# Kernel tuning notes

Measured on AMD Instinct MI355X. Metric: run time of the kernel, lower is better.

Reference implementation:

```python
import jax, jax.numpy as jnp
import numpy as np

N = 50000      # nodes
E = 400000     # edges (before self loops)
F_IN = 128     # num_features
HID = 64       # hidden_dim
HEADS = 4
G = 64         # number of graphs in batch
NCLS = 2
NEG = 0.2      # leaky relu negative slope
BN_EPS = 1e-5


def setup_inputs() -> dict:
    key = jax.random.key(0)
    ks = jax.random.split(key, 32)
    rn = lambda k, shape, s=0.05: jax.random.normal(k, shape, jnp.float32) * s
    inp = {}
    inp["x"] = jax.random.normal(ks[0], (N, F_IN), jnp.float32)
    inp["edge_index"] = jax.random.randint(ks[1], (2, E), 0, N, dtype=jnp.int32)
    inp["batch"] = jnp.sort(jax.random.randint(ks[2], (N,), 0, G, dtype=jnp.int32))
    # layer 0 GATConv (concat=True) + pre projection
    inp["conv0_W"] = rn(ks[3], (F_IN, HEADS * HID))
    inp["conv0_att_src"] = rn(ks[4], (HEADS, HID))
    inp["conv0_att_dst"] = rn(ks[5], (HEADS, HID))
    inp["conv0_bias"] = jnp.zeros((HEADS * HID,), jnp.float32)
    inp["pre0_W"] = rn(ks[6], (HEADS * HID, HID))
    inp["pre0_b"] = jnp.zeros((HID,), jnp.float32)
    # layers 1..2 GATConv (concat=False), stacked
    inp["convs_W"] = rn(ks[7], (2, HID, HEADS * HID))
    inp["convs_att_src"] = rn(ks[8], (2, HEADS, HID))
    inp["convs_att_dst"] = rn(ks[9], (2, HEADS, HID))
    inp["convs_bias"] = jnp.zeros((2, HID), jnp.float32)
    # batch norms (eval mode: running stats)
    inp["bn_gamma"] = jnp.ones((3, HID), jnp.float32)
    inp["bn_beta"] = jnp.zeros((3, HID), jnp.float32)
    inp["bn_mean"] = rn(ks[10], (3, HID), 0.1)
    inp["bn_var"] = jax.random.uniform(ks[11], (3, HID), jnp.float32) + 0.5
    # JK projection, attention pooling, classifier
    inp["jump_W"] = rn(ks[12], (3 * HID, HID))
    inp["jump_b"] = jnp.zeros((HID,), jnp.float32)
    inp["att_W"] = rn(ks[13], (HID, 1))
    inp["att_b"] = jnp.zeros((1,), jnp.float32)
    inp["cls_W1"] = rn(ks[14], (HID, HID // 2))
    inp["cls_b1"] = jnp.zeros((HID // 2,), jnp.float32)
    inp["cls_W2"] = rn(ks[15], (HID // 2, NCLS))
    inp["cls_b2"] = jnp.zeros((NCLS,), jnp.float32)
    return inp


def _segment_softmax(logits, seg, num_segments):
    m = jax.ops.segment_max(logits, seg, num_segments=num_segments)
    e = jnp.exp(logits - m[seg])
    s = jax.ops.segment_sum(e, seg, num_segments=num_segments)
    return e / s[seg]


def _gat_conv(x, src, dst, W, a_src, a_dst, bias, concat):
    n = x.shape[0]
    H, C = a_src.shape
    xh = (x @ W).reshape(n, H, C)                         # [N, H, C]
    as_n = jnp.einsum('nhc,hc->nh', xh, a_src)            # [N, H]
    ad_n = jnp.einsum('nhc,hc->nh', xh, a_dst)            # [N, H]
    logits = jax.nn.leaky_relu(as_n[src] + ad_n[dst], NEG)  # [E', H]
    att = _segment_softmax(logits, dst, n)                # softmax over incoming edges
    out = jax.ops.segment_sum(xh[src] * att[:, :, None], dst, num_segments=n)
    out = out.reshape(n, H * C) if concat else out.mean(axis=1)
    return out + bias


def _bn(h, g, b, m, v):
    return (h - m) * jax.lax.rsqrt(v + BN_EPS) * g + b


def reference(x, edge_index, batch, conv0_W, conv0_att_src, conv0_att_dst,
              conv0_bias, pre0_W, pre0_b, convs_W, convs_att_src, convs_att_dst,
              convs_bias, bn_gamma, bn_beta, bn_mean, bn_var, jump_W, jump_b,
              att_W, att_b, cls_W1, cls_b1, cls_W2, cls_b2):
    n = x.shape[0]
    loops = jnp.arange(n, dtype=edge_index.dtype)
    src = jnp.concatenate([edge_index[0], loops])         # add_self_loops=True
    dst = jnp.concatenate([edge_index[1], loops])
    reps = []
    # layer 0: concat heads -> pre projection -> BN -> ELU (no residual: 128 != 64)
    h = _gat_conv(x, src, dst, conv0_W, conv0_att_src, conv0_att_dst, conv0_bias, True)
    h = h @ pre0_W + pre0_b
    h = jax.nn.elu(_bn(h, bn_gamma[0], bn_beta[0], bn_mean[0], bn_var[0]))
    reps.append(h)
    # layers 1..2: mean heads -> BN -> ELU -> residual
    for i in range(2):
        h_in = h
        h = _gat_conv(h, src, dst, convs_W[i], convs_att_src[i], convs_att_dst[i],
                      convs_bias[i], False)
        h = jax.nn.elu(_bn(h, bn_gamma[i + 1], bn_beta[i + 1], bn_mean[i + 1], bn_var[i + 1]))
        h = h + h_in
        reps.append(h)
    # jumping knowledge (cat)
    h = jnp.concatenate(reps, axis=-1) @ jump_W + jump_b  # [N, HID]
    # attentional global pooling
    a = _segment_softmax((h @ att_W + att_b)[:, 0], batch, G)  # [N]
    hg = jax.ops.segment_sum(h * a[:, None], batch, num_segments=G)  # [G, HID]
    # classifier
    return jax.nn.relu(hg @ cls_W1 + cls_b1) @ cls_W2 + cls_b2
```

## Files before the change

### kernel.cpp

```cpp
#include <hip/hip_runtime.h>
#include <hip/hip_bf16.h>
#include <math.h>

#define NEG 0.2f
#define BNEPS 1e-5f
#define NGRAPH 64
#define SCAN_CHUNK 2048
#define POOL_BLOCKS 256

typedef short bf16x8 __attribute__((ext_vector_type(8)));
typedef float f32x4  __attribute__((ext_vector_type(4)));
typedef float f32x2  __attribute__((ext_vector_type(2)));

__device__ __forceinline__ float bf2f(unsigned short u) {
    return __uint_as_float(((unsigned)u) << 16);
}
__device__ __forceinline__ short f2bf(float f) {
    return (short)__bfloat16_as_ushort(__float2bfloat16(f));
}
__device__ __forceinline__ unsigned char f2fp8(float f) {
    int pk = __builtin_amdgcn_cvt_pk_fp8_f32(f, f, 0, false);
    return (unsigned char)(pk & 0xFF);
}

__global__ __launch_bounds__(256)
void init_kernel(const int* __restrict__ batch, int N,
                 int* __restrict__ counts, int* __restrict__ gstart,
                 float* __restrict__ hg_acc, float* __restrict__ wsum_acc,
                 const float* __restrict__ convs_W,
                 const float* __restrict__ convs_as, const float* __restrict__ convs_ad,
                 float* __restrict__ uv)
{
    int idx = blockIdx.x * 256 + threadIdx.x;
    for (int i = idx; i < N; i += gridDim.x * 256) counts[i] = 0;
    if (blockIdx.x == 0) {
        int t = threadIdx.x;
        for (int i = t; i < NGRAPH * 64; i += 256) hg_acc[i] = 0.f;
        if (t < NGRAPH) wsum_acc[t] = 0.f;
        if (t <= NGRAPH) {
            int lo = 0, hi = N;
            while (lo < hi) {
                int mid = (lo + hi) >> 1;
                if (batch[mid] < t) lo = mid + 1; else hi = mid;
            }
            gstart[t] = lo;
        }
    }
    if (blockIdx.x == 1) {
        int t = threadIdx.x;
        int h = t >> 6, k = t & 63;
        for (int i = 0; i < 2; ++i) {
            const float* Wr  = convs_W + (size_t)i * 64 * 256 + k * 256 + h * 64;
            const float* av  = convs_as + i * 256 + h * 64;
            const float* dv  = convs_ad + i * 256 + h * 64;
            float su = 0.f, sv = 0.f;
            for (int c = 0; c < 64; ++c) { su += Wr[c] * av[c]; sv += Wr[c] * dv[c]; }
            uv[i * 256 + h * 64 + k]       = su;
            uv[512 + i * 256 + h * 64 + k] = sv;
        }
    }
}

__global__ __launch_bounds__(256)
void gemm_xh_mfma(const float* __restrict__ A, int lda,
                  const float* __restrict__ W, int Nc, int M, int K,
                  const float* __restrict__ att_s, const float* __restrict__ att_d,
                  float* __restrict__ as_out, float* __restrict__ ad_out,
                  unsigned char* __restrict__ C8)
{
    __shared__ short Wt[64 * 136];
    const int KP = K + 8;
    int tid  = threadIdx.x;
    int lane = tid & 63, wave = tid >> 6;
    int row0 = blockIdx.x * 64;
    int colb = blockIdx.y * 64;
    int c15 = lane & 15, q = lane >> 4;

    {
        int n = tid & 63;
        for (int k = tid >> 6; k < K; k += 4)
            Wt[n * KP + k] = f2bf(W[(size_t)k * Nc + colb + n]);
    }
    __syncthreads();

    int row = row0 + wave * 16 + c15;
    bool rok = row < M;
    const float* arow = A + (size_t)row * lda + q * 8;

    f32x4 acc[4];
    #pragma unroll
    for (int st = 0; st < 4; ++st) acc[st] = (f32x4){0.f, 0.f, 0.f, 0.f};

    for (int k0 = 0; k0 < K; k0 += 32) {
        bf16x8 av;
        if (rok) {
            float4 a0 = *(const float4*)(arow + k0);
            float4 a1 = *(const float4*)(arow + k0 + 4);
            av[0] = f2bf(a0.x); av[1] = f2bf(a0.y); av[2] = f2bf(a0.z); av[3] = f2bf(a0.w);
            av[4] = f2bf(a1.x); av[5] = f2bf(a1.y); av[6] = f2bf(a1.z); av[7] = f2bf(a1.w);
        } else {
            av = (bf16x8){0,0,0,0,0,0,0,0};
        }
        #pragma unroll
        for (int st = 0; st < 4; ++st) {
            bf16x8 bv = *(const bf16x8*)(Wt + (st * 16 + c15) * KP + k0 + q * 8);
            acc[st] = __builtin_amdgcn_mfma_f32_16x16x32_bf16(av, bv, acc[st], 0, 0, 0);
        }
    }

    #pragma unroll
    for (int r = 0; r < 4; ++r) {
        int orow = row0 + wave * 16 + q * 4 + r;
        if (orow >= M) continue;
        unsigned char* cb = C8 + (size_t)orow * 256 + colb + c15;
        #pragma unroll
        for (int st = 0; st < 4; ++st)
            cb[st * 16] = f2fp8(acc[st][r]);
    }
    float sa[4], da[4];
    #pragma unroll
    for (int st = 0; st < 4; ++st) {
        sa[st] = att_s[colb + st * 16 + c15];
        da[st] = att_d[colb + st * 16 + c15];
    }
    #pragma unroll
    for (int r = 0; r < 4; ++r) {
        float ps = acc[0][r] * sa[0] + acc[1][r] * sa[1] + acc[2][r] * sa[2] + acc[3][r] * sa[3];
        float pd = acc[0][r] * da[0] + acc[1][r] * da[1] + acc[2][r] * da[2] + acc[3][r] * da[3];
        #pragma unroll
        for (int o = 1; o < 16; o <<= 1) {
            ps += __shfl_xor(ps, o);
            pd += __shfl_xor(pd, o);
        }
        int orow = row0 + wave * 16 + q * 4 + r;
        if (c15 == 0 && orow < M) {
            as_out[orow * 4 + blockIdx.y] = ps;
            ad_out[orow * 4 + blockIdx.y] = pd;
        }
    }
}

__global__ __launch_bounds__(256)
void gemm_n64_mfma(const void* __restrict__ Araw, int lda, int a_is_bf16,
                   const float* __restrict__ W, int w_gat, int M, int K,
                   const float* __restrict__ bias, float scale,
                   float* __restrict__ C, int ldc, int mode,
                   const float* __restrict__ bn_g, const float* __restrict__ bn_b,
                   const float* __restrict__ bn_m, const float* __restrict__ bn_v,
                   const float* __restrict__ resid, int ldr,
                   unsigned char* __restrict__ h8_out,
                   const float* __restrict__ u, const float* __restrict__ v,
                   float* __restrict__ as_out, float* __restrict__ ad_out,
                   const float* __restrict__ attW, const float* __restrict__ attb,
                   float* __restrict__ wout)
{
    __shared__ short Wt[64 * 264];
    const int KP = K + 8;
    int tid  = threadIdx.x;
    int lane = tid & 63, wave = tid >> 6;
    int row0 = blockIdx.x * 64;
    int c15 = lane & 15, q = lane >> 4;

    {
        int n = tid & 63;
        for (int k = tid >> 6; k < K; k += 4) {
            int widx = w_gat ? ((k & 63) * 256 + (k >> 6) * 64 + n) : (k * 64 + n);
            Wt[n * KP + k] = f2bf(W[widx]);
        }
    }
    __syncthreads();

    int row = row0 + wave * 16 + c15;
    bool rok = row < M;

    f32x4 acc[4];
    #pragma unroll
    for (int st = 0; st < 4; ++st) acc[st] = (f32x4){0.f, 0.f, 0.f, 0.f};

    for (int k0 = 0; k0 < K; k0 += 32) {
        bf16x8 av;
        if (rok) {
            if (a_is_bf16) {
                av = *(const bf16x8*)((const unsigned short*)Araw
                                      + (size_t)row * lda + k0 + q * 8);
            } else {
                const float* ap = (const float*)Araw + (size_t)row * lda + k0 + q * 8;
                float4 a0 = *(const float4*)ap;
                float4 a1 = *(const float4*)(ap + 4);
                av[0] = f2bf(a0.x); av[1] = f2bf(a0.y); av[2] = f2bf(a0.z); av[3] = f2bf(a0.w);
                av[4] = f2bf(a1.x); av[5] = f2bf(a1.y); av[6] = f2bf(a1.z); av[7] = f2bf(a1.w);
            }
        } else {
            av = (bf16x8){0,0,0,0,0,0,0,0};
        }
        #pragma unroll
        for (int st = 0; st < 4; ++st) {
            bf16x8 bv = *(const bf16x8*)(Wt + (st * 16 + c15) * KP + k0 + q * 8);
            acc[st] = __builtin_amdgcn_mfma_f32_16x16x32_bf16(av, bv, acc[st], 0, 0, 0);
        }
    }

    #pragma unroll
    for (int st = 0; st < 4; ++st) {
        int col = st * 16 + c15;
        float bs = bias ? bias[col] : 0.f;
        float sg = 1.f, sb = 0.f;
        if (mode == 1) {
            sg = bn_g[col] / sqrtf(bn_v[col] + BNEPS);
            sb = bn_b[col] - bn_m[col] * sg;
        }
        #pragma unroll
        for (int r = 0; r < 4; ++r) {
            int orow = row0 + wave * 16 + q * 4 + r;
            if (orow >= M) continue;
            float vvv = acc[st][r] * scale + bs;
            if (mode == 1) {
                vvv = vvv * sg + sb;
                vvv = vvv > 0.f ? vvv : __expf(vvv) - 1.f;
            }
            if (resid) vvv += resid[(size_t)orow * ldr + col];
            acc[st][r] = vvv;
            C[(size_t)orow * ldc + col] = vvv;
        }
    }

    if (h8_out) {
        #pragma unroll
        for (int r = 0; r < 4; ++r) {
            int orow = row0 + wave * 16 + q * 4 + r;
            if (orow >= M) continue;
            unsigned char* hb = h8_out + (size_t)orow * 64 + c15;
            #pragma unroll
            for (int st = 0; st < 4; ++st)
                hb[st * 16] = f2fp8(acc[st][r]);
        }
    }

    if (u) {
        float uu[4][4], vv2[4][4];
        #pragma unroll
        for (int h = 0; h < 4; ++h)
            #pragma unroll
            for (int st = 0; st < 4; ++st) {
                uu[h][st]  = u[h * 64 + st * 16 + c15];
                vv2[h][st] = v[h * 64 + st * 16 + c15];
            }
        #pragma unroll
        for (int r = 0; r < 4; ++r) {
            int orow = row0 + wave * 16 + q * 4 + r;
            float pv[8];
            #pragma unroll
            for (int h = 0; h < 4; ++h) {
                pv[h]     = acc[0][r] * uu[h][0] + acc[1][r] * uu[h][1]
                          + acc[2][r] * uu[h][2] + acc[3][r] * uu[h][3];
                pv[4 + h] = acc[0][r] * vv2[h][0] + acc[1][r] * vv2[h][1]
                          + acc[2][r] * vv2[h][2] + acc[3][r] * vv2[h][3];
            }
            #pragma unroll
            for (int jj = 0; jj < 8; ++jj)
                #pragma unroll
                for (int o = 1; o < 16; o <<= 1) pv[jj] += __shfl_xor(pv[jj], o);
            if (c15 == 0 && orow < M) {
                #pragma unroll
                for (int h = 0; h < 4; ++h) {
                    as_out[orow * 4 + h] = pv[h];
                    ad_out[orow * 4 + h] = pv[4 + h];
                }
            }
        }
    }

    if (wout) {
        float sa[4];
        #pragma unroll
        for (int st = 0; st < 4; ++st) sa[st] = attW[st * 16 + c15];
        float ab = attb[0];
        #pragma unroll
        for (int r = 0; r < 4; ++r) {
            float ps = acc[0][r] * sa[0] + acc[1][r] * sa[1]
                     + acc[2][r] * sa[2] + acc[3][r] * sa[3];
            #pragma unroll
            for (int o = 1; o < 16; o <<= 1) ps += __shfl_xor(ps, o);
            int orow = row0 + wave * 16 + q * 4 + r;
            if (c15 == 0 && orow < M) wout[orow] = __expf(ps + ab);
        }
    }
}

__global__ __launch_bounds__(256)
void hist_kernel(const int* __restrict__ ei, int E, int N, int* __restrict__ counts)
{
    int e = blockIdx.x * blockDim.x + threadIdx.x;
    int Etot = E + N;
    if (e >= Etot) return;
    int d = (e < E) ? ei[E + e] : e - E;
    atomicAdd(&counts[d], 1);
}

__global__ __launch_bounds__(256)
void scan_phase1(const int* __restrict__ counts, int N, int* __restrict__ blocksum)
{
    __shared__ int wsum[4];
    int tid = threadIdx.x, lane = tid & 63, wave = tid >> 6;
    int base = blockIdx.x * SCAN_CHUNK;
    int s = 0;
    #pragma unroll
    for (int j = 0; j < SCAN_CHUNK / 256; ++j) {
        int idx = base + tid + j * 256;
        if (idx < N) s += counts[idx];
    }
    #pragma unroll
    for (int o = 32; o; o >>= 1) s += __shfl_xor(s, o);
    if (lane == 0) wsum[wave] = s;
    __syncthreads();
    if (tid == 0) blocksum[blockIdx.x] = wsum[0] + wsum[1] + wsum[2] + wsum[3];
}

__global__ __launch_bounds__(256)
void scan_phase3(const int* __restrict__ counts, int N, int nb,
                 const int* __restrict__ blocksum,
                 int* __restrict__ rowptr, int* __restrict__ cursor)
{
    __shared__ int wsum[4];
    __shared__ int pref[64];
    int tid = threadIdx.x, lane = tid & 63, wave = tid >> 6;

    if (wave == 0) {
        int v = (lane < nb) ? blocksum[lane] : 0;
        int incl = v;
        #pragma unroll
        for (int o = 1; o < 64; o <<= 1) {
            int t = __shfl_up(incl, o);
            if (lane >= o) incl += t;
        }
        pref[lane] = incl;
    }
    __syncthreads();
    int boff = blockIdx.x ? pref[blockIdx.x - 1] : 0;
    if (blockIdx.x == 0 && tid == 0) rowptr[N] = pref[nb - 1];

    int start = blockIdx.x * SCAN_CHUNK + tid * 8;
    int v[8];
    int s = 0;
    #pragma unroll
    for (int j = 0; j < 8; ++j) {
        v[j] = (start + j < N) ? counts[start + j] : 0;
        s += v[j];
    }
    int incl = s;
    #pragma unroll
    for (int o = 1; o < 64; o <<= 1) {
        int t = __shfl_up(incl, o);
        if (lane >= o) incl += t;
    }
    if (lane == 63) wsum[wave] = incl;
    __syncthreads();
    int woff = 0;
    #pragma unroll
    for (int w = 0; w < 4; ++w) if (w < wave) woff += wsum[w];
    int run = boff + woff + incl - s;
    #pragma unroll
    for (int j = 0; j < 8; ++j) {
        int idx = start + j;
        if (idx < N) { rowptr[idx] = run; cursor[idx] = run; }
        run += v[j];
    }
}

__global__ __launch_bounds__(256)
void scatter_kernel(const int* __restrict__ ei, int E, int N,
                    int* __restrict__ cursor, int* __restrict__ csr_src)
{
    int e = blockIdx.x * blockDim.x + threadIdx.x;
    int Etot = E + N;
    if (e >= Etot) return;
    int s, d;
    if (e < E) { s = ei[e]; d = ei[E + e]; } else { s = d = e - E; }
    int pos = atomicAdd(&cursor[d], 1);
    csr_src[pos] = s;
}

__global__ __launch_bounds__(256)
void aggregate_kernel(const int* __restrict__ rowptr, const int* __restrict__ csr_src,
                      const float* __restrict__ as_n, const float* __restrict__ ad_n,
                      const unsigned char* __restrict__ xh8,
                      const float* __restrict__ bias,
                      unsigned short* __restrict__ outp, int N)
{
    int node = (blockIdx.x * blockDim.x + threadIdx.x) >> 6;
    int lane = threadIdx.x & 63;
    if (node >= N) return;
    int h = lane >> 4, li = lane & 15, grp = lane & 48;
    int e0 = rowptr[node], e1 = rowptr[node + 1];
    float adh = ad_n[node * 4 + h];
    unsigned laneoff = (unsigned)(lane * 4);

    float4 acc = make_float4(0.f, 0.f, 0.f, 0.f);
    float wsum = 0.f;

    for (int base = e0; base < e1; base += 16) {
        int cnt = e1 - base; if (cnt > 16) cnt = 16;
        int s = 0; float w = 0.f;
        if (li < cnt) {
            s = csr_src[base + li];
            float l = as_n[s * 4 + h] + adh;
            l = fmaxf(l, NEG * l);
            w = __expf(l);
        }
        int k = 0;
        for (; k + 3 < cnt; k += 4) {
            float w0 = __shfl(w, grp + k),     w1 = __shfl(w, grp + k + 1);
            float w2 = __shfl(w, grp + k + 2), w3 = __shfl(w, grp + k + 3);
            int s0 = __shfl(s, grp + k),       s1 = __shfl(s, grp + k + 1);
            int s2 = __shfl(s, grp + k + 2),   s3 = __shfl(s, grp + k + 3);
            unsigned x0 = *(const unsigned*)(xh8 + ((unsigned)s0 * 256u + laneoff));
            unsigned x1 = *(const unsigned*)(xh8 + ((unsigned)s1 * 256u + laneoff));
            unsigned x2 = *(const unsigned*)(xh8 + ((unsigned)s2 * 256u + laneoff));
            unsigned x3 = *(const unsigned*)(xh8 + ((unsigned)s3 * 256u + laneoff));
            f32x2 l0 = __builtin_amdgcn_cvt_pk_f32_fp8((int)x0, false);
            f32x2 h0 = __builtin_amdgcn_cvt_pk_f32_fp8((int)x0, true);
            f32x2 l1 = __builtin_amdgcn_cvt_pk_f32_fp8((int)x1, false);
            f32x2 h1 = __builtin_amdgcn_cvt_pk_f32_fp8((int)x1, true);
            f32x2 l2 = __builtin_amdgcn_cvt_pk_f32_fp8((int)x2, false);
            f32x2 h2 = __builtin_amdgcn_cvt_pk_f32_fp8((int)x2, true);
            f32x2 l3 = __builtin_amdgcn_cvt_pk_f32_fp8((int)x3, false);
            f32x2 h3 = __builtin_amdgcn_cvt_pk_f32_fp8((int)x3, true);
            acc.x += w0 * l0.x; acc.y += w0 * l0.y; acc.z += w0 * h0.x; acc.w += w0 * h0.y;
            acc.x += w1 * l1.x; acc.y += w1 * l1.y; acc.z += w1 * h1.x; acc.w += w1 * h1.y;
            acc.x += w2 * l2.x; acc.y += w2 * l2.y; acc.z += w2 * h2.x; acc.w += w2 * h2.y;
            acc.x += w3 * l3.x; acc.y += w3 * l3.y; acc.z += w3 * h3.x; acc.w += w3 * h3.y;
            wsum += (w0 + w1) + (w2 + w3);
        }
        for (; k < cnt; ++k) {
            float wk = __shfl(w, grp + k);
            int sk = __shfl(s, grp + k);
            unsigned xv = *(const unsigned*)(xh8 + ((unsigned)sk * 256u + laneoff));
            f32x2 lo = __builtin_amdgcn_cvt_pk_f32_fp8((int)xv, false);
            f32x2 hi = __builtin_amdgcn_cvt_pk_f32_fp8((int)xv, true);
            acc.x += wk * lo.x; acc.y += wk * lo.y;
            acc.z += wk * hi.x; acc.w += wk * hi.y;
            wsum += wk;
        }
    }

    float rw = 1.f / wsum;
    float4 bs = *(const float4*)(bias + lane * 4);
    ushort4 pk;
    pk.x = (unsigned short)f2bf(acc.x * rw + bs.x);
    pk.y = (unsigned short)f2bf(acc.y * rw + bs.y);
    pk.z = (unsigned short)f2bf(acc.z * rw + bs.z);
    pk.w = (unsigned short)f2bf(acc.w * rw + bs.w);
    *(ushort4*)(outp + (size_t)node * 256 + lane * 4) = pk;
}

__global__ __launch_bounds__(256)
void aggregate_z(const int* __restrict__ rowptr, const int* __restrict__ csr_src,
                 const float* __restrict__ as_n, const float* __restrict__ ad_n,
                 const unsigned char* __restrict__ h8,
                 unsigned short* __restrict__ zout, int N)
{
    int node = (blockIdx.x * blockDim.x + threadIdx.x) >> 6;
    int lane = threadIdx.x & 63;
    if (node >= N) return;
    int g = lane >> 4, li = lane & 15, grp = lane & 48;
    int e0 = rowptr[node], e1 = rowptr[node + 1];
    float adh = ad_n[node * 4 + g];

    float acc[4][4];
    #pragma unroll
    for (int h = 0; h < 4; ++h)
        #pragma unroll
        for (int j = 0; j < 4; ++j) acc[h][j] = 0.f;
    float wsum = 0.f;

    for (int base = e0; base < e1; base += 16) {
        int cnt = e1 - base; if (cnt > 16) cnt = 16;
        int s = 0; float w = 0.f;
        if (li < cnt) {
            s = csr_src[base + li];
            float l = as_n[s * 4 + g] + adh;
            l = fmaxf(l, NEG * l);
            w = __expf(l);
        }
        wsum += w;
        for (int k = 0; k < cnt; k += 4) {
            int m = k + g;
            int   sm = __shfl(s, grp + m);
            float w0 = __shfl(w, m);
            float w1 = __shfl(w, 16 + m);
            float w2 = __shfl(w, 32 + m);
            float w3 = __shfl(w, 48 + m);
            if (m < cnt) {
                unsigned xv = *(const unsigned*)(h8 + ((unsigned)sm * 64u + (unsigned)(li * 4)));
                f32x2 lo = __builtin_amdgcn_cvt_pk_f32_fp8((int)xv, false);
                f32x2 hi = __builtin_amdgcn_cvt_pk_f32_fp8((int)xv, true);
                float f0 = lo.x, f1 = lo.y, f2 = hi.x, f3 = hi.y;
                acc[0][0] += w0 * f0; acc[0][1] += w0 * f1; acc[0][2] += w0 * f2; acc[0][3] += w0 * f3;
                acc[1][0] += w1 * f0; acc[1][1] += w1 * f1; acc[1][2] += w1 * f2; acc[1][3] += w1 * f3;
                acc[2][0] += w2 * f0; acc[2][1] += w2 * f1; acc[2][2] += w2 * f2; acc[2][3] += w2 * f3;
                acc[3][0] += w3 * f0; acc[3][1] += w3 * f1; acc[3][2] += w3 * f2; acc[3][3] += w3 * f3;
            }
        }
    }

    #pragma unroll
    for (int o = 1; o < 16; o <<= 1) wsum += __shfl_xor(wsum, o);
    #pragma unroll
    for (int h = 0; h < 4; ++h)
        #pragma unroll
        for (int j = 0; j < 4; ++j) {
            acc[h][j] += __shfl_xor(acc[h][j], 16);
            acc[h][j] += __shfl_xor(acc[h][j], 32);
        }
    float rw = 1.f / wsum;
    ushort4 pk;
    pk.x = (unsigned short)f2bf(acc[g][0] * rw);
    pk.y = (unsigned short)f2bf(acc[g][1] * rw);
    pk.z = (unsigned short)f2bf(acc[g][2] * rw);
    pk.w = (unsigned short)f2bf(acc[g][3] * rw);
    *(ushort4*)(zout + (size_t)node * 256 + g * 64 + li * 4) = pk;
}

__global__ __launch_bounds__(256)
void pool_partial(const float* __restrict__ hjk, const float* __restrict__ w,
                  const int* __restrict__ batch, const int* __restrict__ gstart,
                  float* __restrict__ hg_acc, float* __restrict__ wsum_acc, int N)
{
    __shared__ float red[256];
    __shared__ float wred[4];
    int tid = threadIdx.x;
    int c = tid & 63, q = tid >> 6;
    int slab = (N + POOL_BLOCKS - 1) / POOL_BLOCKS;
    int n0 = blockIdx.x * slab;
    int n1 = n0 + slab; if (n1 > N) n1 = N;
    if (n0 >= n1) return;
    int g0 = batch[n0], g1 = batch[n1 - 1];

    for (int g = g0; g <= g1; ++g) {
        int s = gstart[g];     if (s < n0) s = n0;
        int e = gstart[g + 1]; if (e > n1) e = n1;
        float acc = 0.f, ws = 0.f;
        for (int n = s + q; n < e; n += 4) {
            float wn = w[n];
            acc += wn * hjk[(size_t)n * 64 + c];
            if (c == 0) ws += wn;
        }
        red[tid] = acc;
        if (c == 0) wred[q] = ws;
        __syncthreads();
        if (q == 0) {
            float v = red[c] + red[64 + c] + red[128 + c] + red[192 + c];
            if (v != 0.f) atomicAdd(&hg_acc[g * 64 + c], v);
            if (c == 0) {
                float t = wred[0] + wred[1] + wred[2] + wred[3];
                if (t != 0.f) atomicAdd(&wsum_acc[g], t);
            }
        }
        __syncthreads();
    }
}

__global__ void cls_kernel(const float* __restrict__ hg_acc,
                           const float* __restrict__ wsum_acc,
                           const float* __restrict__ W1, const float* __restrict__ b1,
                           const float* __restrict__ W2, const float* __restrict__ b2,
                           float* __restrict__ out)
{
    int g = blockIdx.x, t = threadIdx.x;
    __shared__ float z[32];
    __shared__ float h[64];
    float wsum = wsum_acc[g];
    float rw = (wsum > 0.f) ? 1.f / wsum : 0.f;
    h[t] = hg_acc[g * 64 + t] * rw;
    h[t + 32] = hg_acc[g * 64 + t + 32] * rw;
    __syncthreads();
    float acc = b1[t];
    for (int k = 0; k < 64; ++k) acc += h[k] * W1[k * 32 + t];
    z[t] = fmaxf(acc, 0.f);
    __syncthreads();
    if (t < 2) {
        float o = b2[t];
        for (int j = 0; j < 32; ++j) o += z[j] * W2[j * 2 + t];
        out[g * 2 + t] = o;
    }
}

extern "C" void kernel_launch(void* const* d_in, const int* in_sizes, int n_in,
                              void* d_out, int out_size, void* d_ws, size_t ws_size,
                              hipStream_t stream)
{
    const float* x        = (const float*)d_in[0];
    const int*   ei       = (const int*)d_in[1];
    const int*   batch    = (const int*)d_in[2];
    const float* conv0_W  = (const float*)d_in[3];
    const float* conv0_as = (const float*)d_in[4];
    const float* conv0_ad = (const float*)d_in[5];
    const float* conv0_b  = (const float*)d_in[6];
    const float* pre0_W   = (const float*)d_in[7];
    const float* pre0_b   = (const float*)d_in[8];
    const float* convs_W  = (const float*)d_in[9];
    const float* convs_as = (const float*)d_in[10];
    const float* convs_ad = (const float*)d_in[11];
    const float* convs_b  = (const float*)d_in[12];
    const float* bn_g     = (const float*)d_in[13];
    const float* bn_b     = (const float*)d_in[14];
    const float* bn_m     = (const float*)d_in[15];
    const float* bn_v     = (const float*)d_in[16];
    const float* jump_W   = (const float*)d_in[17];
    const float* jump_b   = (const float*)d_in[18];
    const float* att_W    = (const float*)d_in[19];
    const float* att_b    = (const float*)d_in[20];
    const float* cls_W1   = (const float*)d_in[21];
    const float* cls_b1   = (const float*)d_in[22];
    const float* cls_W2   = (const float*)d_in[23];
    const float* cls_b2   = (const float*)d_in[24];
    float* out = (float*)d_out;

    const int N = in_sizes[0] / 128;
    const int E = in_sizes[1] / 2;
    const int Etot = E + N;
    const int nb = (N + SCAN_CHUNK - 1) / SCAN_CHUNK;

    float* ws      = (float*)d_ws;
    unsigned char* xh8      = (unsigned char*)ws;
    unsigned short* h256_bf = (unsigned short*)ws + (size_t)N * 256;
    float* repsAll = (float*)(h256_bf + (size_t)N * 256);
    float* as_n    = repsAll + (size_t)N * 192;
    float* ad_n    = as_n + (size_t)N * 4;
    float* hjk     = ad_n + (size_t)N * 4;
    float* hg_acc  = hjk + (size_t)N * 64;
    float* wsum_acc= hg_acc + NGRAPH * 64;
    int*   rowptr  = (int*)(wsum_acc + NGRAPH);
    int*   cursor  = rowptr + (N + 1);
    int*   counts  = cursor + N;
    int*   csr_src = counts + N;
    int*   gstart  = csr_src + Etot;
    int*   blocksum = gstart + (NGRAPH + 1);
    float* uv      = (float*)(blocksum + 64);
    unsigned char* h8 = xh8;
    float* wbuf    = as_n;

    dim3 blk(256);
    int node_wave_blocks = (N + 3) / 4;
    int edge_blocks      = (Etot + 255) / 256;
    int row_blocks       = (N + 63) / 64;

    init_kernel<<<64, blk, 0, stream>>>(batch, N, counts, gstart, hg_acc, wsum_acc,
                                        convs_W, convs_as, convs_ad, uv);
    hist_kernel<<<edge_blocks, blk, 0, stream>>>(ei, E, N, counts);
    scan_phase1<<<nb, blk, 0, stream>>>(counts, N, blocksum);
    scan_phase3<<<nb, blk, 0, stream>>>(counts, N, nb, blocksum, rowptr, cursor);
    scatter_kernel<<<edge_blocks, blk, 0, stream>>>(ei, E, N, cursor, csr_src);

    {
        dim3 g1(row_blocks, 4);
        gemm_xh_mfma<<<g1, blk, 0, stream>>>(x, 128, conv0_W, 256, N, 128,
                                             conv0_as, conv0_ad, as_n, ad_n, xh8);
        aggregate_kernel<<<node_wave_blocks, blk, 0, stream>>>(
            rowptr, csr_src, as_n, ad_n, xh8, conv0_b, h256_bf, N);
        gemm_n64_mfma<<<row_blocks, blk, 0, stream>>>(
            h256_bf, 256, 1, pre0_W, 0, N, 256, pre0_b, 1.f,
            repsAll, 192, 1, bn_g, bn_b, bn_m, bn_v,
            nullptr, 0, h8, uv, uv + 512, as_n, ad_n,
            nullptr, nullptr, nullptr);
    }

    aggregate_z<<<node_wave_blocks, blk, 0, stream>>>(rowptr, csr_src, as_n, ad_n,
                                                      h8, h256_bf, N);
    gemm_n64_mfma<<<row_blocks, blk, 0, stream>>>(
        h256_bf, 256, 1, convs_W, 1, N, 256, convs_b, 0.25f,
        repsAll + 64, 192, 1, bn_g + 64, bn_b + 64, bn_m + 64, bn_v + 64,
        repsAll, 192, h8, uv + 256, uv + 512 + 256, as_n, ad_n,
        nullptr, nullptr, nullptr);

    aggregate_z<<<node_wave_blocks, blk, 0, stream>>>(rowptr, csr_src, as_n, ad_n,
                                                      h8, h256_bf, N);
    gemm_n64_mfma<<<row_blocks, blk, 0, stream>>>(
        h256_bf, 256, 1, convs_W + (size_t)64 * 256, 1, N, 256, convs_b + 64, 0.25f,
        repsAll + 128, 192, 1, bn_g + 128, bn_b + 128, bn_m + 128, bn_v + 128,
        repsAll + 64, 192, nullptr, nullptr, nullptr, nullptr, nullptr,
        nullptr, nullptr, nullptr);

    gemm_n64_mfma<<<row_blocks, blk, 0, stream>>>(
        repsAll, 192, 0, jump_W, 0, N, 192, jump_b, 1.f,
        hjk, 64, 0, nullptr, nullptr, nullptr, nullptr,
        nullptr, 0, nullptr, nullptr, nullptr, nullptr, nullptr,
        att_W, att_b, wbuf);

    pool_partial<<<POOL_BLOCKS, blk, 0, stream>>>(hjk, wbuf, batch, gstart,
                                                  hg_acc, wsum_acc, N);
    cls_kernel<<<NGRAPH, 32, 0, stream>>>(hg_acc, wsum_acc, cls_W1, cls_b1,
                                          cls_W2, cls_b2, out);
}
```

Measured before the change: 394.5 us.

## Restructure aggregate_z to per-head lane groups and reduce attention dot shuffles

The aggregation kernel now gives each 16-lane group one head. Every group walks all edges with the same source rows, unrolled by four, so no cross-group accumulator reduction is needed and the register footprint drops from 16 accumulators to 4. In exchange each group issues four times as many gathers per edge and runs a serial per-edge loop. Separately, the GEMM epilogue replaces eight full 16-lane butterfly reductions with a recursive-halving transpose-reduce that leaves each lane holding one of the eight attention sums. This cuts the shuffle count in that epilogue.

```diff
diff --git a/kernel.cpp b/kernel.cpp
--- a/kernel.cpp
+++ b/kernel.cpp
@@ -257,15 +257,27 @@
                           + acc[2][r] * vv2[h][2] + acc[3][r] * vv2[h][3];
             }
             #pragma unroll
-            for (int jj = 0; jj < 8; ++jj)
-                #pragma unroll
-                for (int o = 1; o < 16; o <<= 1) pv[jj] += __shfl_xor(pv[jj], o);
-            if (c15 == 0 && orow < M) {
-                #pragma unroll
-                for (int h = 0; h < 4; ++h) {
-                    as_out[orow * 4 + h] = pv[h];
-                    ad_out[orow * 4 + h] = pv[4 + h];
-                }
+            for (int j = 0; j < 4; ++j) {
+                float send = (c15 & 8) ? pv[j] : pv[j + 4];
+                float keep = (c15 & 8) ? pv[j + 4] : pv[j];
+                pv[j] = keep + __shfl_xor(send, 8);
+            }
+            #pragma unroll
+            for (int j = 0; j < 2; ++j) {
+                float send = (c15 & 4) ? pv[j] : pv[j + 2];
+                float keep = (c15 & 4) ? pv[j + 2] : pv[j];
+                pv[j] = keep + __shfl_xor(send, 4);
+            }
+            {
+                float send = (c15 & 2) ? pv[0] : pv[1];
+                float keep = (c15 & 2) ? pv[1] : pv[0];
+                pv[0] = keep + __shfl_xor(send, 2);
+            }
+            pv[0] += __shfl_xor(pv[0], 1);
+            if ((c15 & 1) == 0 && orow < M) {
+                int jj = c15 >> 1;
+                if (jj < 4) as_out[orow * 4 + jj] = pv[0];
+                else        ad_out[orow * 4 + (jj - 4)] = pv[0];
             }
         }
     }
@@ -462,15 +474,12 @@
     int node = (blockIdx.x * blockDim.x + threadIdx.x) >> 6;
     int lane = threadIdx.x & 63;
     if (node >= N) return;
-    int g = lane >> 4, li = lane & 15, grp = lane & 48;
+    int h = lane >> 4, li = lane & 15, grp = lane & 48;
     int e0 = rowptr[node], e1 = rowptr[node + 1];
-    float adh = ad_n[node * 4 + g];
-
-    float acc[4][4];
-    #pragma unroll
-    for (int h = 0; h < 4; ++h)
-        #pragma unroll
-        for (int j = 0; j < 4; ++j) acc[h][j] = 0.f;
+    float adh = ad_n[node * 4 + h];
+    unsigned laneoff = (unsigned)(li * 4);
+
+    float4 acc = make_float4(0.f, 0.f, 0.f, 0.f);
     float wsum = 0.f;
 
     for (int base = e0; base < e1; base += 16) {
@@ -478,47 +487,53 @@
         int s = 0; float w = 0.f;
         if (li < cnt) {
             s = csr_src[base + li];
-            float l = as_n[s * 4 + g] + adh;
+            float l = as_n[s * 4 + h] + adh;
             l = fmaxf(l, NEG * l);
             w = __expf(l);
         }
-        wsum += w;
-        for (int k = 0; k < cnt; k += 4) {
-            int m = k + g;
-            int   sm = __shfl(s, grp + m);
-            float w0 = __shfl(w, m);
-            float w1 = __shfl(w, 16 + m);
-            float w2 = __shfl(w, 32 + m);
-            float w3 = __shfl(w, 48 + m);
-            if (m < cnt) {
-                unsigned xv = *(const unsigned*)(h8 + ((unsigned)sm * 64u + (unsigned)(li * 4)));
-                f32x2 lo = __builtin_amdgcn_cvt_pk_f32_fp8((int)xv, false);
-                f32x2 hi = __builtin_amdgcn_cvt_pk_f32_fp8((int)xv, true);
-                float f0 = lo.x, f1 = lo.y, f2 = hi.x, f3 = hi.y;
-                acc[0][0] += w0 * f0; acc[0][1] += w0 * f1; acc[0][2] += w0 * f2; acc[0][3] += w0 * f3;
-                acc[1][0] += w1 * f0; acc[1][1] += w1 * f1; acc[1][2] += w1 * f2; acc[1][3] += w1 * f3;
-                acc[2][0] += w2 * f0; acc[2][1] += w2 * f1; acc[2][2] += w2 * f2; acc[2][3] += w2 * f3;
-                acc[3][0] += w3 * f0; acc[3][1] += w3 * f1; acc[3][2] += w3 * f2; acc[3][3] += w3 * f3;
-            }
-        }
-    }
-
-    #pragma unroll
-    for (int o = 1; o < 16; o <<= 1) wsum += __shfl_xor(wsum, o);
-    #pragma unroll
-    for (int h = 0; h < 4; ++h)
-        #pragma unroll
-        for (int j = 0; j < 4; ++j) {
-            acc[h][j] += __shfl_xor(acc[h][j], 16);
-            acc[h][j] += __shfl_xor(acc[h][j], 32);
-        }
+        int k = 0;
+        for (; k + 3 < cnt; k += 4) {
+            float w0 = __shfl(w, grp + k),     w1 = __shfl(w, grp + k + 1);
+            float w2 = __shfl(w, grp + k + 2), w3 = __shfl(w, grp + k + 3);
+            int s0 = __shfl(s, grp + k),       s1 = __shfl(s, grp + k + 1);
+            int s2 = __shfl(s, grp + k + 2),   s3 = __shfl(s, grp + k + 3);
+            unsigned x0 = *(const unsigned*)(h8 + ((unsigned)s0 * 64u + laneoff));
+            unsigned x1 = *(const unsigned*)(h8 + ((unsigned)s1 * 64u + laneoff));
+            unsigned x2 = *(const unsigned*)(h8 + ((unsigned)s2 * 64u + laneoff));
+            unsigned x3 = *(const unsigned*)(h8 + ((unsigned)s3 * 64u + laneoff));
+            f32x2 l0 = __builtin_amdgcn_cvt_pk_f32_fp8((int)x0, false);
+            f32x2 h0 = __builtin_amdgcn_cvt_pk_f32_fp8((int)x0, true);
+            f32x2 l1 = __builtin_amdgcn_cvt_pk_f32_fp8((int)x1, false);
+            f32x2 h1 = __builtin_amdgcn_cvt_pk_f32_fp8((int)x1, true);
+            f32x2 l2 = __builtin_amdgcn_cvt_pk_f32_fp8((int)x2, false);
+            f32x2 h2 = __builtin_amdgcn_cvt_pk_f32_fp8((int)x2, true);
+            f32x2 l3 = __builtin_amdgcn_cvt_pk_f32_fp8((int)x3, false);
+            f32x2 h3 = __builtin_amdgcn_cvt_pk_f32_fp8((int)x3, true);
+            acc.x += w0 * l0.x; acc.y += w0 * l0.y; acc.z += w0 * h0.x; acc.w += w0 * h0.y;
+            acc.x += w1 * l1.x; acc.y += w1 * l1.y; acc.z += w1 * h1.x; acc.w += w1 * h1.y;
+            acc.x += w2 * l2.x; acc.y += w2 * l2.y; acc.z += w2 * h2.x; acc.w += w2 * h2.y;
+            acc.x += w3 * l3.x; acc.y += w3 * l3.y; acc.z += w3 * h3.x; acc.w += w3 * h3.y;
+            wsum += (w0 + w1) + (w2 + w3);
+        }
+        for (; k < cnt; ++k) {
+            float wk = __shfl(w, grp + k);
+            int sk = __shfl(s, grp + k);
+            unsigned xv = *(const unsigned*)(h8 + ((unsigned)sk * 64u + laneoff));
+            f32x2 lo = __builtin_amdgcn_cvt_pk_f32_fp8((int)xv, false);
+            f32x2 hi = __builtin_amdgcn_cvt_pk_f32_fp8((int)xv, true);
+            acc.x += wk * lo.x; acc.y += wk * lo.y;
+            acc.z += wk * hi.x; acc.w += wk * hi.y;
+            wsum += wk;
+        }
+    }
+
     float rw = 1.f / wsum;
     ushort4 pk;
-    pk.x = (unsigned short)f2bf(acc[g][0] * rw);
-    pk.y = (unsigned short)f2bf(acc[g][1] * rw);
-    pk.z = (unsigned short)f2bf(acc[g][2] * rw);
-    pk.w = (unsigned short)f2bf(acc[g][3] * rw);
-    *(ushort4*)(zout + (size_t)node * 256 + g * 64 + li * 4) = pk;
+    pk.x = (unsigned short)f2bf(acc.x * rw);
+    pk.y = (unsigned short)f2bf(acc.y * rw);
+    pk.z = (unsigned short)f2bf(acc.z * rw);
+    pk.w = (unsigned short)f2bf(acc.w * rw);
+    *(ushort4*)(zout + (size_t)node * 256 + h * 64 + li * 4) = pk;
 }
 
 __global__ __launch_bounds__(256)
```

After: 366.2 us. 1.08x faster.
